# Kernel tuning notes

Hardware: AMD Instinct MI355X
Metric: run time of the kernel (lower is better)

The kernel has to match this reference:

```python
import jax, jax.numpy as jnp
import numpy as np

N_NODES = 50000
N_EDGES = 1600000
IN_CH = 128
HID_CH = 128
OUT_CH = 2
NUM_GRAPHS = 64
NUM_LAYERS = 3


def setup_inputs() -> dict:
    key = jax.random.key(0)
    ks = jax.random.split(key, 12)
    x = jax.random.normal(ks[0], (N_NODES, IN_CH), dtype=jnp.float32)
    edge_index = jax.random.randint(ks[1], (2, N_EDGES), 0, N_NODES, dtype=jnp.int64)
    batch = jnp.sort(jax.random.randint(ks[2], (N_NODES,), 0, NUM_GRAPHS, dtype=jnp.int64))
    s = 0.05
    W0 = jax.random.normal(ks[3], (IN_CH, HID_CH), dtype=jnp.float32) * s
    b0 = jnp.zeros((HID_CH,), dtype=jnp.float32)
    W1 = jax.random.normal(ks[4], (HID_CH, HID_CH), dtype=jnp.float32) * s
    b1 = jnp.zeros((HID_CH,), dtype=jnp.float32)
    W2 = jax.random.normal(ks[5], (HID_CH, HID_CH), dtype=jnp.float32) * s
    b2 = jnp.zeros((HID_CH,), dtype=jnp.float32)
    Wlin = jax.random.normal(ks[6], (HID_CH, OUT_CH), dtype=jnp.float32) * s
    blin = jnp.zeros((OUT_CH,), dtype=jnp.float32)
    return {"x": x, "edge_index": edge_index, "batch": batch,
            "W0": W0, "b0": b0, "W1": W1, "b1": b1, "W2": W2, "b2": b2,
            "Wlin": Wlin, "blin": blin}


def _gcn_layer(h, src, dst, norm, W, b):
    # GCNConv: (D^-1/2 (A+I) D^-1/2) (h W) + b
    h = h @ W                               # [N, C]
    msg = h[src] * norm[:, None]            # [E+N, C] gather + scale
    agg = jax.ops.segment_sum(msg, dst, num_segments=N_NODES)  # scatter-add
    return agg + b


def reference(x, edge_index, batch, W0, b0, W1, b1, W2, b2, Wlin, blin):
    loops = jnp.arange(N_NODES, dtype=edge_index.dtype)
    src = jnp.concatenate([edge_index[0], loops])
    dst = jnp.concatenate([edge_index[1], loops])
    deg = jax.ops.segment_sum(jnp.ones_like(dst, dtype=x.dtype), dst,
                              num_segments=N_NODES)
    dis = jax.lax.rsqrt(deg)                # deg >= 1 due to self loops
    norm = dis[src] * dis[dst]              # [E+N]

    h = x
    for W, b in ((W0, b0), (W1, b1), (W2, b2)):
        h = jax.nn.relu(_gcn_layer(h, src, dst, norm, W, b))

    # global mean pool over graphs
    sums = jax.ops.segment_sum(h, batch, num_segments=NUM_GRAPHS)
    cnts = jax.ops.segment_sum(jnp.ones((N_NODES,), dtype=h.dtype), batch,
                               num_segments=NUM_GRAPHS)
    pooled = sums / jnp.maximum(cnts, 1.0)[:, None]  # [G, HID]
    return pooled @ Wlin + blin                       # [G, OUT]
```

## Files before the change

kernel.cpp:

```cpp
#include <hip/hip_runtime.h>
#include <hip/hip_fp16.h>

#define N_NODES   50000
#define N_EDGES   1600000
#define CH        128
#define OUTC      2
#define NGRAPHS   64

#define NBUCK     391
#define EPB       4096
#define F1BLOCKS  391
#define BCAP      5120

#define GR        64

using f16x8 = __attribute__((ext_vector_type(8))) _Float16;
using f32x4 = __attribute__((ext_vector_type(4))) float;


__global__ __launch_bounds__(256) void bhist_k(const int* __restrict__ dst,
                                               int* __restrict__ bhist) {
    __shared__ int hist[NBUCK];
    const int tid = threadIdx.x;
    const int e0  = blockIdx.x * EPB;
    const int nE  = min(EPB, N_EDGES - e0);
    for (int i = tid; i < NBUCK; i += 256) hist[i] = 0;
    __syncthreads();
    for (int i = tid; i < nE; i += 256) atomicAdd(&hist[dst[e0 + i] >> 7], 1);
    __syncthreads();
    for (int i = tid; i < NBUCK; i += 256) if (hist[i]) atomicAdd(&bhist[i], hist[i]);
}

__global__ __launch_bounds__(512) void bscan_k(const int* __restrict__ bhist,
                                               int* __restrict__ bbase,
                                               int* __restrict__ bcur) {
    const int t = threadIdx.x, lane = t & 63, w = t >> 6;
    int v = (t < NBUCK) ? bhist[t] : 0;
    int iv = v;
    #pragma unroll
    for (int d = 1; d < 64; d <<= 1) {
        int o = __shfl_up(iv, d, 64);
        if (lane >= d) iv += o;
    }
    __shared__ int ws[8];
    if (lane == 63) ws[w] = iv;
    __syncthreads();
    int add = 0;
    #pragma unroll
    for (int k = 0; k < 8; k++) if (k < w) add += ws[k];
    int excl = add + iv - v;
    if (t < NBUCK) { bbase[t] = excl; bcur[t] = excl; }
    if (t == NBUCK - 1) bbase[NBUCK] = excl + v;
}

__global__ __launch_bounds__(256) void bucket_scatter_k(const int* __restrict__ src,
                                                        const int* __restrict__ dst,
                                                        int* __restrict__ bucketCursor,
                                                        int2* __restrict__ stage) {
    __shared__ int hist[NBUCK];
    __shared__ int cur[NBUCK];
    __shared__ int gbase[NBUCK];
    const int tid = threadIdx.x;
    const int e0  = blockIdx.x * EPB;
    const int nE  = min(EPB, N_EDGES - e0);

    for (int i = tid; i < NBUCK; i += 256) hist[i] = 0;
    __syncthreads();
    for (int i = tid; i < nE; i += 256) {
        int d = dst[e0 + i];
        atomicAdd(&hist[d >> 7], 1);
    }
    __syncthreads();
    for (int i = tid; i < NBUCK; i += 256) {
        int h = hist[i];
        gbase[i] = h ? atomicAdd(&bucketCursor[i], h) : 0;
        cur[i] = 0;
    }
    __syncthreads();
    for (int i = tid; i < nE; i += 256) {
        int d = dst[e0 + i];
        int s = src[e0 + i];
        int b = d >> 7;
        int pos = gbase[b] + atomicAdd(&cur[b], 1);
        stage[pos] = make_int2(s, d);
    }
}

__global__ __launch_bounds__(256) void bucket_build_k(const int2* __restrict__ stage,
                                                      const int* __restrict__ bbase,
                                                      int* __restrict__ offsets,
                                                      float* __restrict__ dis,
                                                      int* __restrict__ csr) {
    __shared__ int lcnt[128];
    __shared__ int lcur[128];
    __shared__ int wtot[2];
    __shared__ int loc[BCAP];
    const int tid    = threadIdx.x;
    const int b      = blockIdx.x;
    const int first  = b << 7;
    const int nNodes = min(128, N_NODES - first);
    const int base   = bbase[b];
    const int bsize  = bbase[b + 1] - base;

    if (tid < 128) lcnt[tid] = 0;
    __syncthreads();
    for (int i = tid; i < bsize; i += 256)
        atomicAdd(&lcnt[stage[base + i].y - first], 1);
    __syncthreads();

    int iv = 0, c = 0;
    if (tid < 128) {
        c = lcnt[tid];
        iv = c;
        #pragma unroll
        for (int d = 1; d < 64; d <<= 1) {
            int o = __shfl_up(iv, d, 64);
            if ((tid & 63) >= d) iv += o;
        }
        if ((tid & 63) == 63) wtot[tid >> 6] = iv;
    }
    __syncthreads();
    if (tid < 128) {
        int add  = (tid >= 64) ? wtot[0] : 0;
        int excl = add + iv - c;
        lcur[tid] = excl;
        if (tid < nNodes) {
            offsets[first + tid] = base + excl;
            dis[first + tid]     = rsqrtf((float)(c + 1));
        }
    }
    if (b == NBUCK - 1 && tid == 0) offsets[N_NODES] = base + bsize;
    __syncthreads();

    if (bsize <= BCAP) {
        for (int i = tid; i < bsize; i += 256) {
            int2 sd = stage[base + i];
            int pos = atomicAdd(&lcur[sd.y - first], 1);
            loc[pos] = sd.x;
        }
        __syncthreads();
        for (int i = tid; i < bsize; i += 256) csr[base + i] = loc[i];
    } else {
        for (int i = tid; i < bsize; i += 256) {
            int2 sd = stage[base + i];
            int pos = atomicAdd(&lcur[sd.y - first], 1);
            csr[base + pos] = sd.x;
        }
    }
}

__global__ __launch_bounds__(256) void boundary_k(const int* __restrict__ batch,
                                                  int* __restrict__ gstart) {
    int i = blockIdx.x * 256 + threadIdx.x;
    if (i >= N_NODES) return;
    int bc = batch[i];
    if (i == 0) {
        for (int g = 0; g <= bc; g++) gstart[g] = 0;
    } else {
        int bp = batch[i - 1];
        for (int g = bp + 1; g <= bc; g++) gstart[g] = i;
    }
    if (i == N_NODES - 1) {
        for (int g = bc + 1; g <= NGRAPHS; g++) gstart[g] = N_NODES;
    }
}

__global__ __launch_bounds__(256) void prep_w_k(const float* __restrict__ W0,
                                                const float* __restrict__ W1,
                                                const float* __restrict__ W2,
                                                __half* __restrict__ T0,
                                                __half* __restrict__ T1,
                                                __half* __restrict__ T2) {
    const float* W = (blockIdx.x == 0) ? W0 : (blockIdx.x == 1) ? W1 : W2;
    __half* Wt     = (blockIdx.x == 0) ? T0 : (blockIdx.x == 1) ? T1 : T2;
    for (int i = threadIdx.x; i < CH * CH; i += 256) {
        int k = i >> 7, c = i & 127;
        Wt[c * CH + k] = __float2half(W[i]);
    }
}

template <bool F32IN>
__global__ __launch_bounds__(256) void gemm_mfma_k(const void* __restrict__ hin,
                                                   const __half* __restrict__ Wt,
                                                   const float* __restrict__ dis,
                                                   __half* __restrict__ out) {
    __shared__ _Float16 Hl[GR][136];
    __shared__ _Float16 Wl[CH][136];
    const int tid = threadIdx.x;
    const int rowBase = blockIdx.x * GR;

    {
        const int c = tid >> 1, q = tid & 1;
        #pragma unroll
        for (int i = 0; i < 8; i++)
            *(f16x8*)&Wl[c][q * 64 + i * 8] =
                *(const f16x8*)&Wt[c * CH + q * 64 + i * 8];
    }
    {
        const int r = tid >> 2, q = tid & 3;
        const int n = rowBase + r;
        if constexpr (F32IN) {
            const float* h = (const float*)hin;
            #pragma unroll
            for (int i = 0; i < 8; i++) {
                float4 v = make_float4(0.f, 0.f, 0.f, 0.f);
                if (n < N_NODES) v = *(const float4*)&h[(size_t)n * CH + q * 32 + i * 4];
                *(__half2*)&Hl[r][q * 32 + i * 4]     = __floats2half2_rn(v.x, v.y);
                *(__half2*)&Hl[r][q * 32 + i * 4 + 2] = __floats2half2_rn(v.z, v.w);
            }
        } else {
            const _Float16* h = (const _Float16*)hin;
            #pragma unroll
            for (int i = 0; i < 4; i++) {
                f16x8 v = {};
                if (n < N_NODES) v = *(const f16x8*)&h[(size_t)n * CH + q * 32 + i * 8];
                *(f16x8*)&Hl[r][q * 32 + i * 8] = v;
            }
        }
    }
    __syncthreads();

    const int w = tid >> 6, lane = tid & 63;
    const int l15 = lane & 15, kg = lane >> 4;

    f32x4 acc[8];
    #pragma unroll
    for (int t = 0; t < 8; t++) acc[t] = (f32x4){0.f, 0.f, 0.f, 0.f};

    #pragma unroll
    for (int kt = 0; kt < 4; kt++) {
        f16x8 a = *(f16x8*)&Hl[w * 16 + l15][kt * 32 + kg * 8];
        #pragma unroll
        for (int t = 0; t < 8; t++) {
            f16x8 b = *(f16x8*)&Wl[t * 16 + l15][kt * 32 + kg * 8];
            acc[t] = __builtin_amdgcn_mfma_f32_16x16x32_f16(a, b, acc[t], 0, 0, 0);
        }
    }
    __syncthreads();

    #pragma unroll
    for (int r = 0; r < 4; r++) {
        const int lrow = w * 16 + kg * 4 + r;
        const int n = rowBase + lrow;
        const float s = (n < N_NODES) ? dis[n] : 0.f;
        #pragma unroll
        for (int t = 0; t < 8; t++)
            Hl[lrow][t * 16 + l15] = (_Float16)(acc[t][r] * s);
    }
    __syncthreads();

    {
        const int r = tid >> 2, q = tid & 3;
        const int n = rowBase + r;
        if (n < N_NODES) {
            #pragma unroll
            for (int i = 0; i < 4; i++)
                *(f16x8*)&((_Float16*)out)[(size_t)n * CH + q * 32 + i * 8] =
                    *(f16x8*)&Hl[r][q * 32 + i * 8];
        }
    }
}

__global__ __launch_bounds__(256) void agg_k(const __half* __restrict__ hs,
                                             const int* __restrict__ offsets,
                                             const int* __restrict__ csr,
                                             const float* __restrict__ dis,
                                             const float* __restrict__ bias,
                                             __half* __restrict__ out) {
    const __half2* hs2 = (const __half2*)hs;
    const int wid  = threadIdx.x >> 6;
    const int lane = threadIdx.x & 63;
    const int n = blockIdx.x * 4 + wid;
    if (n >= N_NODES) return;

    float ax[8], ay[8];
    #pragma unroll
    for (int j = 0; j < 8; j++) { ax[j] = 0.f; ay[j] = 0.f; }

    {
        float2 v = __half22float2(hs2[(size_t)n * 64 + lane]);
        ax[0] = v.x; ay[0] = v.y;
    }

    const int beg = offsets[n];
    const int end = offsets[n + 1];
    int e = beg;
    for (; e + 8 <= end; e += 8) {
        int idx[8];
        #pragma unroll
        for (int j = 0; j < 8; j++) idx[j] = csr[e + j];
        __half2 v[8];
        #pragma unroll
        for (int j = 0; j < 8; j++) v[j] = hs2[(size_t)idx[j] * 64 + lane];
        #pragma unroll
        for (int j = 0; j < 8; j++) {
            float2 f = __half22float2(v[j]);
            ax[j] += f.x; ay[j] += f.y;
        }
    }
    for (; e < end; e++) {
        int s = csr[e];
        float2 f = __half22float2(hs2[(size_t)s * 64 + lane]);
        ax[0] += f.x; ay[0] += f.y;
    }

    #pragma unroll
    for (int j = 0; j < 4; j++) { ax[j] += ax[j + 4]; ay[j] += ay[j + 4]; }
    #pragma unroll
    for (int j = 0; j < 2; j++) { ax[j] += ax[j + 2]; ay[j] += ay[j + 2]; }
    float sx = ax[0] + ax[1];
    float sy = ay[0] + ay[1];

    const float dn = dis[n];
    float2 b = *(const float2*)&bias[lane * 2];
    float rx = fmaxf(dn * sx + b.x, 0.f);
    float ry = fmaxf(dn * sy + b.y, 0.f);
    ((__half2*)out)[(size_t)n * 64 + lane] = __floats2half2_rn(rx, ry);
}

__global__ __launch_bounds__(256) void pool_k(const __half* __restrict__ h,
                                              const int* __restrict__ gstart,
                                              float* __restrict__ gsum) {
    const __half2* h2 = (const __half2*)h;
    const int g   = blockIdx.y;
    const int s   = blockIdx.x;
    const int tid = threadIdx.x;
    const int r   = tid >> 5;
    const int cq  = tid & 31;
    const int start = gstart[g], end = gstart[g + 1];
    const int len   = end - start;
    const int chunk = (len + 7) >> 3;
    const int lo = start + s * chunk;
    const int hi = min(lo + chunk, end);

    float4 acc = make_float4(0.f, 0.f, 0.f, 0.f);
    for (int row = lo + r; row < hi; row += 8) {
        float2 a = __half22float2(h2[(size_t)row * 64 + cq * 2]);
        float2 b = __half22float2(h2[(size_t)row * 64 + cq * 2 + 1]);
        acc.x += a.x; acc.y += a.y; acc.z += b.x; acc.w += b.y;
    }

    __shared__ float4 red[256];
    red[tid] = acc;
    __syncthreads();
    #pragma unroll
    for (int off = 4; off >= 1; off >>= 1) {
        if (r < off) {
            float4 o = red[tid + off * 32];
            red[tid].x += o.x; red[tid].y += o.y;
            red[tid].z += o.z; red[tid].w += o.w;
        }
        __syncthreads();
    }
    if (r == 0) {
        float4 v = red[tid];
        atomicAdd(&gsum[g * CH + cq * 4 + 0], v.x);
        atomicAdd(&gsum[g * CH + cq * 4 + 1], v.y);
        atomicAdd(&gsum[g * CH + cq * 4 + 2], v.z);
        atomicAdd(&gsum[g * CH + cq * 4 + 3], v.w);
    }
}

__global__ __launch_bounds__(128) void head_k(const float* __restrict__ gsum,
                                              const int* __restrict__ gstart,
                                              const float* __restrict__ Wlin,
                                              const float* __restrict__ blin,
                                              float* __restrict__ out) {
    const int t = threadIdx.x;
    const int g = t >> 1;
    const int o = t & 1;
    float cnt = (float)max(gstart[g + 1] - gstart[g], 1);
    float s = 0.f;
    for (int ci = 0; ci < CH; ci++) s += gsum[g * CH + ci] * Wlin[ci * OUTC + o];
    out[g * OUTC + o] = s / cnt + blin[o];
}


static inline size_t alignup(size_t x) { return (x + 255) & ~(size_t)255; }

extern "C" void kernel_launch(void* const* d_in, const int* in_sizes, int n_in,
                              void* d_out, int out_size, void* d_ws, size_t ws_size,
                              hipStream_t stream) {
    const float* x     = (const float*)d_in[0];
    const int*   eidx  = (const int*)d_in[1];
    const int*   batch = (const int*)d_in[2];
    const float* W0    = (const float*)d_in[3];
    const float* b0    = (const float*)d_in[4];
    const float* W1    = (const float*)d_in[5];
    const float* b1    = (const float*)d_in[6];
    const float* W2    = (const float*)d_in[7];
    const float* b2    = (const float*)d_in[8];
    const float* Wlin  = (const float*)d_in[9];
    const float* blin  = (const float*)d_in[10];
    float* out = (float*)d_out;

    const int* src = eidx;
    const int* dst = eidx + N_EDGES;

    char* p = (char*)d_ws;
    int*    offsets = (int*)p;     p += alignup((N_NODES + 1) * 4);
    float*  dis     = (float*)p;   p += alignup(N_NODES * 4);
    int*    bhist   = (int*)p;     p += alignup(NBUCK * 4);
    int*    bbase   = (int*)p;     p += alignup((NBUCK + 1) * 4);
    int*    bcur    = (int*)p;     p += alignup(NBUCK * 4);
    int*    gstart  = (int*)p;     p += alignup((NGRAPHS + 1) * 4);
    int*    csr     = (int*)p;     p += alignup((size_t)N_EDGES * 4);
    __half* Wt0     = (__half*)p;  p += alignup(CH * CH * 2);
    __half* Wt1     = (__half*)p;  p += alignup(CH * CH * 2);
    __half* Wt2     = (__half*)p;  p += alignup(CH * CH * 2);
    __half* bufA    = (__half*)p;  p += alignup((size_t)N_NODES * CH * 2);
    __half* hsbuf   = (__half*)p;  p += alignup((size_t)N_NODES * CH * 2);
    int2*   stage   = (int2*)p;    p += alignup((size_t)N_EDGES * 8);
    float*  gsum    = (float*)p;   p += alignup(NGRAPHS * CH * 4);

    hipMemsetAsync(bhist, 0, NBUCK * 4, stream);
    hipMemsetAsync(gsum, 0, NGRAPHS * CH * 4, stream);

    bhist_k<<<F1BLOCKS, 256, 0, stream>>>(dst, bhist);
    bscan_k<<<1, 512, 0, stream>>>(bhist, bbase, bcur);
    bucket_scatter_k<<<F1BLOCKS, 256, 0, stream>>>(src, dst, bcur, stage);
    bucket_build_k<<<NBUCK, 256, 0, stream>>>(stage, bbase, offsets, dis, csr);
    boundary_k<<<(N_NODES + 255) / 256, 256, 0, stream>>>(batch, gstart);
    prep_w_k<<<3, 256, 0, stream>>>(W0, W1, W2, Wt0, Wt1, Wt2);

    const int GB = (N_NODES + GR - 1) / GR;
    const int AB = (N_NODES + 3) / 4;

    gemm_mfma_k<true><<<GB, 256, 0, stream>>>(x, Wt0, dis, hsbuf);
    agg_k<<<AB, 256, 0, stream>>>(hsbuf, offsets, csr, dis, b0, bufA);
    gemm_mfma_k<false><<<GB, 256, 0, stream>>>(bufA, Wt1, dis, hsbuf);
    agg_k<<<AB, 256, 0, stream>>>(hsbuf, offsets, csr, dis, b1, bufA);
    gemm_mfma_k<false><<<GB, 256, 0, stream>>>(bufA, Wt2, dis, hsbuf);
    agg_k<<<AB, 256, 0, stream>>>(hsbuf, offsets, csr, dis, b2, bufA);

    pool_k<<<dim3(8, NGRAPHS), 256, 0, stream>>>(bufA, gstart, gsum);
    head_k<<<1, 128, 0, stream>>>(gsum, gstart, Wlin, blin, out);
}
```

Before: 307.5 us.

## Split node features into channel slabs and pack edge staging into 32-bit words

Node feature buffers become four channel slabs of 32 halves each. The aggregation kernel launches one grid slice per slab and each wave handles four edges at once with 16 lanes per edge, so each slab (about 3.2MB) is more likely to stay in cache during the random gathers. The GEMM and pool kernels are changed to read and write the slab layout. Edge staging now packs the source index and the local destination into one int instead of an int2, which halves staging traffic. The packing assumes source ids fit in 16 bits, and N_NODES is 50000, so this holds only because node ids stay below 65536.

Result: slower. 450.0 us (+46.3%).

```diff
diff --git a/kernel.cpp b/kernel.cpp
--- a/kernel.cpp
+++ b/kernel.cpp
@@ -13,6 +13,8 @@
 #define BCAP      5120
 
 #define GR        64
+#define NSLAB     4
+#define SLABH2    ((size_t)N_NODES * 16)
 
 using f16x8 = __attribute__((ext_vector_type(8))) _Float16;
 using f32x4 = __attribute__((ext_vector_type(4))) float;
@@ -56,7 +58,7 @@
 __global__ __launch_bounds__(256) void bucket_scatter_k(const int* __restrict__ src,
                                                         const int* __restrict__ dst,
                                                         int* __restrict__ bucketCursor,
-                                                        int2* __restrict__ stage) {
+                                                        int* __restrict__ stage) {
     __shared__ int hist[NBUCK];
     __shared__ int cur[NBUCK];
     __shared__ int gbase[NBUCK];
@@ -82,11 +84,11 @@
         int s = src[e0 + i];
         int b = d >> 7;
         int pos = gbase[b] + atomicAdd(&cur[b], 1);
-        stage[pos] = make_int2(s, d);
-    }
-}
-
-__global__ __launch_bounds__(256) void bucket_build_k(const int2* __restrict__ stage,
+        stage[pos] = s | ((d & 127) << 16);
+    }
+}
+
+__global__ __launch_bounds__(256) void bucket_build_k(const int* __restrict__ stage,
                                                       const int* __restrict__ bbase,
                                                       int* __restrict__ offsets,
                                                       float* __restrict__ dis,
@@ -105,7 +107,7 @@
     if (tid < 128) lcnt[tid] = 0;
     __syncthreads();
     for (int i = tid; i < bsize; i += 256)
-        atomicAdd(&lcnt[stage[base + i].y - first], 1);
+        atomicAdd(&lcnt[((unsigned)stage[base + i]) >> 16], 1);
     __syncthreads();
 
     int iv = 0, c = 0;
@@ -134,17 +136,17 @@
 
     if (bsize <= BCAP) {
         for (int i = tid; i < bsize; i += 256) {
-            int2 sd = stage[base + i];
-            int pos = atomicAdd(&lcur[sd.y - first], 1);
-            loc[pos] = sd.x;
+            int sd = stage[base + i];
+            int pos = atomicAdd(&lcur[((unsigned)sd) >> 16], 1);
+            loc[pos] = sd & 0xFFFF;
         }
         __syncthreads();
         for (int i = tid; i < bsize; i += 256) csr[base + i] = loc[i];
     } else {
         for (int i = tid; i < bsize; i += 256) {
-            int2 sd = stage[base + i];
-            int pos = atomicAdd(&lcur[sd.y - first], 1);
-            csr[base + pos] = sd.x;
+            int sd = stage[base + i];
+            int pos = atomicAdd(&lcur[((unsigned)sd) >> 16], 1);
+            csr[base + pos] = sd & 0xFFFF;
         }
     }
 }
@@ -209,11 +211,11 @@
                 *(__half2*)&Hl[r][q * 32 + i * 4 + 2] = __floats2half2_rn(v.z, v.w);
             }
         } else {
-            const _Float16* h = (const _Float16*)hin;
+            const _Float16* h = (const _Float16*)hin + (size_t)q * N_NODES * 32;
             #pragma unroll
             for (int i = 0; i < 4; i++) {
                 f16x8 v = {};
-                if (n < N_NODES) v = *(const f16x8*)&h[(size_t)n * CH + q * 32 + i * 8];
+                if (n < N_NODES) v = *(const f16x8*)&h[(size_t)n * 32 + i * 8];
                 *(f16x8*)&Hl[r][q * 32 + i * 8] = v;
             }
         }
@@ -253,10 +255,10 @@
         const int r = tid >> 2, q = tid & 3;
         const int n = rowBase + r;
         if (n < N_NODES) {
+            _Float16* o = (_Float16*)out + (size_t)q * N_NODES * 32;
             #pragma unroll
             for (int i = 0; i < 4; i++)
-                *(f16x8*)&((_Float16*)out)[(size_t)n * CH + q * 32 + i * 8] =
-                    *(f16x8*)&Hl[r][q * 32 + i * 8];
+                *(f16x8*)&o[(size_t)n * 32 + i * 8] = *(f16x8*)&Hl[r][q * 32 + i * 8];
         }
     }
 }
@@ -267,66 +269,62 @@
                                              const float* __restrict__ dis,
                                              const float* __restrict__ bias,
                                              __half* __restrict__ out) {
-    const __half2* hs2 = (const __half2*)hs;
+    const int p    = blockIdx.y;
     const int wid  = threadIdx.x >> 6;
     const int lane = threadIdx.x & 63;
     const int n = blockIdx.x * 4 + wid;
     if (n >= N_NODES) return;
-
-    float ax[8], ay[8];
-    #pragma unroll
-    for (int j = 0; j < 8; j++) { ax[j] = 0.f; ay[j] = 0.f; }
-
-    {
-        float2 v = __half22float2(hs2[(size_t)n * 64 + lane]);
-        ax[0] = v.x; ay[0] = v.y;
+    const int eg = lane >> 4;
+    const int d  = lane & 15;
+    const __half2* slab = (const __half2*)hs + (size_t)p * SLABH2;
+
+    float2 acc = make_float2(0.f, 0.f);
+    if (eg == 0) {
+        float2 v = __half22float2(slab[(size_t)n * 16 + d]);
+        acc.x = v.x; acc.y = v.y;
     }
 
     const int beg = offsets[n];
     const int end = offsets[n + 1];
-    int e = beg;
-    for (; e + 8 <= end; e += 8) {
-        int idx[8];
-        #pragma unroll
-        for (int j = 0; j < 8; j++) idx[j] = csr[e + j];
-        __half2 v[8];
-        #pragma unroll
-        for (int j = 0; j < 8; j++) v[j] = hs2[(size_t)idx[j] * 64 + lane];
-        #pragma unroll
-        for (int j = 0; j < 8; j++) {
-            float2 f = __half22float2(v[j]);
-            ax[j] += f.x; ay[j] += f.y;
-        }
-    }
-    for (; e < end; e++) {
-        int s = csr[e];
-        float2 f = __half22float2(hs2[(size_t)s * 64 + lane]);
-        ax[0] += f.x; ay[0] += f.y;
-    }
-
-    #pragma unroll
-    for (int j = 0; j < 4; j++) { ax[j] += ax[j + 4]; ay[j] += ay[j + 4]; }
-    #pragma unroll
-    for (int j = 0; j < 2; j++) { ax[j] += ax[j + 2]; ay[j] += ay[j + 2]; }
-    float sx = ax[0] + ax[1];
-    float sy = ay[0] + ay[1];
-
-    const float dn = dis[n];
-    float2 b = *(const float2*)&bias[lane * 2];
-    float rx = fmaxf(dn * sx + b.x, 0.f);
-    float ry = fmaxf(dn * sy + b.y, 0.f);
-    ((__half2*)out)[(size_t)n * 64 + lane] = __floats2half2_rn(rx, ry);
+    const int last = end - 1;
+    for (int e = beg; e < end; e += 16) {
+        int t0 = e + eg, t1 = e + 4 + eg, t2 = e + 8 + eg, t3 = e + 12 + eg;
+        int i0 = csr[min(t0, last)];
+        int i1 = csr[min(t1, last)];
+        int i2 = csr[min(t2, last)];
+        int i3 = csr[min(t3, last)];
+        __half2 v0 = slab[(size_t)i0 * 16 + d];
+        __half2 v1 = slab[(size_t)i1 * 16 + d];
+        __half2 v2 = slab[(size_t)i2 * 16 + d];
+        __half2 v3 = slab[(size_t)i3 * 16 + d];
+        if (t0 < end) { float2 f = __half22float2(v0); acc.x += f.x; acc.y += f.y; }
+        if (t1 < end) { float2 f = __half22float2(v1); acc.x += f.x; acc.y += f.y; }
+        if (t2 < end) { float2 f = __half22float2(v2); acc.x += f.x; acc.y += f.y; }
+        if (t3 < end) { float2 f = __half22float2(v3); acc.x += f.x; acc.y += f.y; }
+    }
+
+    acc.x += __shfl_xor(acc.x, 16); acc.y += __shfl_xor(acc.y, 16);
+    acc.x += __shfl_xor(acc.x, 32); acc.y += __shfl_xor(acc.y, 32);
+
+    if (eg == 0) {
+        const float dn = dis[n];
+        float2 b = *(const float2*)&bias[p * 32 + d * 2];
+        float rx = fmaxf(dn * acc.x + b.x, 0.f);
+        float ry = fmaxf(dn * acc.y + b.y, 0.f);
+        ((__half2*)out)[(size_t)p * SLABH2 + (size_t)n * 16 + d] = __floats2half2_rn(rx, ry);
+    }
 }
 
 __global__ __launch_bounds__(256) void pool_k(const __half* __restrict__ h,
                                               const int* __restrict__ gstart,
                                               float* __restrict__ gsum) {
-    const __half2* h2 = (const __half2*)h;
     const int g   = blockIdx.y;
     const int s   = blockIdx.x;
     const int tid = threadIdx.x;
     const int r   = tid >> 5;
     const int cq  = tid & 31;
+    const __half2* slab = (const __half2*)h + (size_t)(cq >> 3) * SLABH2;
+    const int dw = (cq & 7) * 2;
     const int start = gstart[g], end = gstart[g + 1];
     const int len   = end - start;
     const int chunk = (len + 7) >> 3;
@@ -335,8 +333,8 @@
 
     float4 acc = make_float4(0.f, 0.f, 0.f, 0.f);
     for (int row = lo + r; row < hi; row += 8) {
-        float2 a = __half22float2(h2[(size_t)row * 64 + cq * 2]);
-        float2 b = __half22float2(h2[(size_t)row * 64 + cq * 2 + 1]);
+        float2 a = __half22float2(slab[(size_t)row * 16 + dw]);
+        float2 b = __half22float2(slab[(size_t)row * 16 + dw + 1]);
         acc.x += a.x; acc.y += a.y; acc.z += b.x; acc.w += b.y;
     }
 
@@ -410,7 +408,7 @@
     __half* Wt2     = (__half*)p;  p += alignup(CH * CH * 2);
     __half* bufA    = (__half*)p;  p += alignup((size_t)N_NODES * CH * 2);
     __half* hsbuf   = (__half*)p;  p += alignup((size_t)N_NODES * CH * 2);
-    int2*   stage   = (int2*)p;    p += alignup((size_t)N_EDGES * 8);
+    int*    stage   = (int*)p;     p += alignup((size_t)N_EDGES * 4);
     float*  gsum    = (float*)p;   p += alignup(NGRAPHS * CH * 4);
 
     hipMemsetAsync(bhist, 0, NBUCK * 4, stream);
@@ -427,11 +425,11 @@
     const int AB = (N_NODES + 3) / 4;
 
     gemm_mfma_k<true><<<GB, 256, 0, stream>>>(x, Wt0, dis, hsbuf);
-    agg_k<<<AB, 256, 0, stream>>>(hsbuf, offsets, csr, dis, b0, bufA);
+    agg_k<<<dim3(AB, NSLAB), 256, 0, stream>>>(hsbuf, offsets, csr, dis, b0, bufA);
     gemm_mfma_k<false><<<GB, 256, 0, stream>>>(bufA, Wt1, dis, hsbuf);
-    agg_k<<<AB, 256, 0, stream>>>(hsbuf, offsets, csr, dis, b1, bufA);
+    agg_k<<<dim3(AB, NSLAB), 256, 0, stream>>>(hsbuf, offsets, csr, dis, b1, bufA);
     gemm_mfma_k<false><<<GB, 256, 0, stream>>>(bufA, Wt2, dis, hsbuf);
-    agg_k<<<AB, 256, 0, stream>>>(hsbuf, offsets, csr, dis, b2, bufA);
+    agg_k<<<dim3(AB, NSLAB), 256, 0, stream>>>(hsbuf, offsets, csr, dis, b2, bufA);
 
     pool_k<<<dim3(8, NGRAPHS), 256, 0, stream>>>(bufA, gstart, gsum);
     head_k<<<1, 128, 0, stream>>>(gsum, gstart, Wlin, blin, out);
```
